# Performance work log

Hardware: AMD Instinct MI355X
Metric: run time of the kernel (lower is better)

## Reference

```python
import jax, jax.numpy as jnp
import numpy as np

# dims
B, T1, T2, SEG = 4, 16, 16, 4          # batch, src len, tgt len, max segment length
V, E, H, ENC = 8000, 256, 256, 512     # vocab, embed, lstm hidden, encoder units
EOS = 2                                 # end-of-segment symbol ($)
NEG = -1e30                             # finite -inf (grad-safe)


def setup_inputs():
    key = jax.random.key(0)
    ks = jax.random.split(key, 16)
    s = 0.05
    n = lambda k, shp: (jax.random.normal(k, shp) * s).astype(jnp.float32)
    return {
        "prev_output_tokens": jax.random.randint(ks[0], (B, T2), 0, V),
        "encoder_outs": jax.random.normal(ks[1], (T1, B, ENC), dtype=jnp.float32),
        "embed": n(ks[2], (V, E)),
        "start_embed": n(ks[3], (E,)),
        "proj_h_w": n(ks[4], (H, ENC)), "proj_h_b": jnp.zeros((H,), jnp.float32),
        "proj_c_w": n(ks[5], (H, ENC)), "proj_c_b": jnp.zeros((H,), jnp.float32),
        "w_ih0": n(ks[6], (4 * H, H + E)), "w_hh0": n(ks[7], (4 * H, H)), "b0": jnp.zeros((4 * H,), jnp.float32),
        "w_ih1": n(ks[8], (4 * H, H)), "w_hh1": n(ks[9], (4 * H, H)), "b1": jnp.zeros((4 * H,), jnp.float32),
        "fc_w": n(ks[10], (V, H)), "fc_b": jnp.zeros((V,), jnp.float32),
    }


def _lstm_cell(x, h, c, w_ih, w_hh, b):
    # PyTorch LSTMCell gate order: i, f, g, o
    g = x @ w_ih.T + h @ w_hh.T + b
    i, f, gg, o = jnp.split(g, 4, axis=-1)
    c_new = jax.nn.sigmoid(f) * c + jax.nn.sigmoid(i) * jnp.tanh(gg)
    h_new = jax.nn.sigmoid(o) * jnp.tanh(c_new)
    return h_new, c_new


def reference(prev_output_tokens, encoder_outs, embed, start_embed,
              proj_h_w, proj_h_b, proj_c_w, proj_c_b,
              w_ih0, w_hh0, b0, w_ih1, w_hh1, b1, fc_w, fc_b):
    y = prev_output_tokens                                     # [B, T2]
    # segment windows: tok[b, t2, k] = y[b, t2+k] (clipped; masked later via logpy mask)
    pos = jnp.arange(T2 + 1)[:, None] + jnp.arange(SEG)[None, :]   # [T2+1, SEG]
    tok = y[:, jnp.minimum(pos, T2 - 1)]                            # [B, T2+1, SEG]
    emb_tok = embed[tok]                                            # [B, T2+1, SEG, E]
    x0 = jnp.broadcast_to(start_embed, (B, T2 + 1, 1, E))
    xs = jnp.moveaxis(jnp.concatenate([x0, emb_tok], axis=2), 2, 0)  # [SEG+1, B, T2+1, E]
    tgt = jnp.concatenate([tok, jnp.zeros((B, T2 + 1, 1), tok.dtype)], axis=2)
    tgt = jnp.moveaxis(tgt, 2, 0)                                    # [SEG+1, B, T2+1]

    # per-encoder-position initial states / context (encoder proj, as in __init__)
    eo = jnp.swapaxes(encoder_outs, 0, 1)                            # [B, T1, ENC]
    h0 = eo @ proj_h_w.T + proj_h_b                                  # [B, T1, H]
    c0 = eo @ proj_c_w.T + proj_c_b
    ctx = jnp.broadcast_to(h0[:, :, None, :], (B, T1, T2 + 1, H))

    def step(carry, inp):
        h1, c1, h2, c2 = carry
        x, t = inp                                                   # x [B,T2+1,E], t [B,T2+1]
        xb = jnp.broadcast_to(x[:, None, :, :], (B, T1, T2 + 1, E))
        h1, c1 = _lstm_cell(jnp.concatenate([ctx, xb], axis=-1), h1, c1, w_ih0, w_hh0, b0)
        h2, c2 = _lstm_cell(h1, h2, c2, w_ih1, w_hh1, b1)
        logp = jax.nn.log_softmax(h2 @ fc_w.T + fc_b, axis=-1)       # [B,T1,T2+1,V]
        idx = jnp.broadcast_to(t[:, None, :, None], (B, T1, T2 + 1, 1))
        sel = jnp.take_along_axis(logp, idx, axis=-1)[..., 0]
        return (h1, c1, h2, c2), (sel, logp[..., EOS])

    carry0 = (ctx,
              jnp.broadcast_to(c0[:, :, None, :], (B, T1, T2 + 1, H)),
              jnp.zeros((B, T1, T2 + 1, H), jnp.float32),
              jnp.zeros((B, T1, T2 + 1, H), jnp.float32))
    _, (sel, eosp) = jax.lax.scan(step, carry0, (xs, tgt))           # each [SEG+1,B,T1,T2+1]

    # logpy[b,t1,t2,j] = sum_{k<j} logp_k(y[t2+k]) + logp_j(EOS)
    cum = jnp.concatenate([jnp.zeros((1, B, T1, T2 + 1), sel.dtype),
                           jnp.cumsum(sel[:SEG], axis=0)], axis=0)
    logpy = jnp.moveaxis(cum + eosp, 0, -1)                          # [B,T1,T2+1,SEG+1]
    jmask = (jnp.arange(T2 + 1)[:, None] + jnp.arange(SEG + 1)[None, :]) <= T2
    logpy = jnp.where(jmask[None, None], logpy, NEG)

    # semi-Markov forward DP: alpha[t1+1, t2] = LSE_j alpha[t1, t2-j] + logpy[t1, t2-j, j]
    alpha0 = jnp.full((B, T2 + 1), NEG, sel.dtype).at[:, 0].set(0.0)

    def dp(alpha, row):                                              # row [B, T2+1, SEG+1]
        v = alpha[:, :, None] + row
        shifted = jnp.stack(
            [jnp.pad(v[:, :T2 + 1 - j, j], ((0, 0), (j, 0)), constant_values=NEG)
             for j in range(SEG + 1)], axis=0)
        return jax.nn.logsumexp(shifted, axis=0), None

    alpha, _ = jax.lax.scan(dp, alpha0, jnp.moveaxis(logpy, 1, 0))
    return alpha[:, T2]                                              # log-likelihood per batch elem
```

## Files before the change

kernel.cpp:

```cpp
#include <hip/hip_runtime.h>
#include <math.h>

#define B 4
#define T1 16
#define T2 16
#define SEG 4
#define V 8000
#define E 256
#define H 256
#define ENC 512
#define EOS 2
#define NEGV -1e30f
#define G4 1024
#define NCELL 1088
#define T21 17
#define NL 272
#define MP 5504
#define NTM 43
#define NTN 63
#define NFCT (NTM*NTN)
#define NPART 126

typedef __attribute__((ext_vector_type(4))) float f32x4;
typedef __attribute__((ext_vector_type(8))) short bf16x8;

__device__ __forceinline__ float sigm(float x) { return 1.f / (1.f + __expf(-x)); }
__device__ __forceinline__ float ftanh(float x) { float e = __expf(2.f * x); return 1.f - 2.f / (e + 1.f); }
__device__ __forceinline__ float b2f(short x) {
    unsigned u = ((unsigned)(unsigned short)x) << 16;
    return __builtin_bit_cast(float, u);
}
__device__ __forceinline__ short f2b(float f) {
    unsigned u = __builtin_bit_cast(unsigned, f);
    unsigned r = (u + 0x7fffu + ((u >> 16) & 1u)) >> 16;
    return (short)r;
}

__device__ __forceinline__ int swz8(int row) { return (row & 7) ^ ((row & 3) << 1); }

__device__ __forceinline__ void stage64(const char* g0, size_t gstrideB, int kOffB, char* lds) {
    int tid = threadIdx.x;
#pragma unroll
    for (int it = 0; it < 8; ++it) {
        int chunk = it * 256 + tid;
        int row = chunk >> 5;
        int g = chunk & 31;
        const char* src = g0 + (size_t)row * gstrideB + kOffB + ((g ^ swz8(row)) << 4);
        __builtin_amdgcn_global_load_lds((const __attribute__((address_space(1))) void*)src,
                                         (__attribute__((address_space(3))) void*)(lds + chunk * 16),
                                         16, 0, 0);
    }
}
__device__ __forceinline__ bf16x8 lds_frag(const char* lds, int row, int col16) {
    return *(const bf16x8*)(lds + row * 512 + ((col16 ^ swz8(row)) << 4));
}
__device__ __forceinline__ void mma_tile(const char* smA, const char* smB,
                                         int wave, int ln, int kg, f32x4 acc[4]) {
#pragma unroll
    for (int ks = 0; ks < 8; ++ks) {
        bf16x8 a = lds_frag(smA, wave * 16 + ln, ks * 4 + kg);
#pragma unroll
        for (int nf = 0; nf < 4; ++nf) {
            bf16x8 b = lds_frag(smB, nf * 16 + ln, ks * 4 + kg);
            acc[nf] = __builtin_amdgcn_mfma_f32_16x16x32_bf16(a, b, acc[nf], 0, 0, 0);
        }
    }
}

__device__ __forceinline__ bf16x8 frag128(const char* lds, int row, int gl) {
    return *(const bf16x8*)(lds + row * 256 + ((gl ^ swz8(row)) << 4));
}

__global__ void k_setup(const float* __restrict__ fcw, const float* __restrict__ whh0,
                        const float* __restrict__ wih1, const float* __restrict__ whh1,
                        const float* __restrict__ phw, const float* __restrict__ pcw,
                        const float* __restrict__ wih0, const float* __restrict__ b1,
                        short* __restrict__ fcwbf, short* __restrict__ whh0i, short* __restrict__ w1i,
                        float* __restrict__ projhT, float* __restrict__ projcT,
                        float* __restrict__ ctxT, float* __restrict__ xT, float* __restrict__ b1i) {
    int bid = blockIdx.x, tid = threadIdx.x;
    if (bid < 2000) {
        int i = (bid * 256 + tid) * 4;
        float4 v = *(const float4*)&fcw[i];
        short4 o = { f2b(v.x), f2b(v.y), f2b(v.z), f2b(v.w) };
        *(short4*)&fcwbf[i] = o;
        return;
    }
    bid -= 2000;
    if (bid < 256) {
        int i = (bid * 256 + tid) * 4;
        int gp = i >> 8, k = i & 255;
        float4 v = *(const float4*)&whh0[(size_t)((gp & 3) * 256 + (gp >> 2)) * 256 + k];
        short4 o = { f2b(v.x), f2b(v.y), f2b(v.z), f2b(v.w) };
        *(short4*)&whh0i[i] = o;
        return;
    }
    bid -= 256;
    if (bid < 512) {
        int i = (bid * 256 + tid) * 4;
        int gp = i >> 9, k = i & 511;
        int g = (gp & 3) * 256 + (gp >> 2);
        const float* src = (k < 256) ? &wih1[(size_t)g * 256 + k] : &whh1[(size_t)g * 256 + (k - 256)];
        float4 v = *(const float4*)src;
        short4 o = { f2b(v.x), f2b(v.y), f2b(v.z), f2b(v.w) };
        *(short4*)&w1i[i] = o;
        return;
    }
    bid -= 512;
    if (bid < 128) {
        int i = (bid * 256 + tid) * 4;
        int k = i >> 8, r = i & 255;
        float4 o = { phw[(size_t)r * ENC + k], phw[(size_t)(r + 1) * ENC + k],
                     phw[(size_t)(r + 2) * ENC + k], phw[(size_t)(r + 3) * ENC + k] };
        *(float4*)&projhT[i] = o;
        return;
    }
    bid -= 128;
    if (bid < 128) {
        int i = (bid * 256 + tid) * 4;
        int k = i >> 8, r = i & 255;
        float4 o = { pcw[(size_t)r * ENC + k], pcw[(size_t)(r + 1) * ENC + k],
                     pcw[(size_t)(r + 2) * ENC + k], pcw[(size_t)(r + 3) * ENC + k] };
        *(float4*)&projcT[i] = o;
        return;
    }
    bid -= 128;
    if (bid < 512) {
        int i = (bid * 256 + tid) * 4;
        int g = i >> 9, k = i & 511;
        float4 v = *(const float4*)&wih0[i];
        float* base = (k < 256) ? &ctxT[(size_t)k * G4 + g] : &xT[(size_t)(k - 256) * G4 + g];
        base[0] = v.x; base[G4] = v.y; base[2 * G4] = v.z; base[3 * G4] = v.w;
        return;
    }
    bid -= 512;
    if (bid < 1) {
        float4 o = { b1[tid], b1[256 + tid], b1[512 + tid], b1[768 + tid] };
        *(float4*)&b1i[tid * 4] = o;
        return;
    }
}

__global__ void k_init_state(const float* __restrict__ enc, const float* __restrict__ phT,
                             const float* __restrict__ phb, const float* __restrict__ pcT,
                             const float* __restrict__ pcb, float* __restrict__ h0, float* __restrict__ c0) {
    __shared__ float eo[ENC];
    int bi = blockIdx.x;
    int b = bi / T1, i = bi % T1;
    int j = threadIdx.x;
    for (int e = j; e < ENC; e += 256) eo[e] = enc[(size_t)(i * B + b) * ENC + e];
    __syncthreads();
    float ha = phb[j], ca = pcb[j];
    for (int e = 0; e < ENC; ++e) {
        float x = eo[e];
        ha += x * phT[(size_t)e * H + j];
        ca += x * pcT[(size_t)e * H + j];
    }
    h0[(size_t)bi * H + j] = ha;
    c0[(size_t)bi * H + j] = ca;
}

__global__ void k_init2(const int* __restrict__ y, const float* __restrict__ embed, const float* __restrict__ se,
                        const float* __restrict__ h0, const float* __restrict__ c0,
                        const float* __restrict__ ctxT, const float* __restrict__ xT,
                        const float* __restrict__ b0,
                        float* __restrict__ c1, float* __restrict__ c2,
                        short* __restrict__ hcA, short* __restrict__ hcB,
                        float* __restrict__ pre_ctxi, float* __restrict__ pre_xi) {
    __shared__ float sb[256];
    int bid = blockIdx.x, j = threadIdx.x;
    if (bid < NCELL) {
        int cell = bid, bi = cell / T21;
        c1[(size_t)cell * H + j] = c0[(size_t)bi * H + j];
        c2[(size_t)cell * H + j] = 0.f;
        hcA[(size_t)cell * 512 + j] = f2b(h0[(size_t)bi * H + j]);
        hcB[(size_t)cell * 512 + 256 + j] = 0;
        return;
    }
    bid -= NCELL;
    if (bid < 64) {
        int bi = bid;
        sb[j] = h0[(size_t)bi * H + j];
        __syncthreads();
        float a0 = b0[j], a1 = b0[256 + j], a2 = b0[512 + j], a3 = b0[768 + j];
        for (int k = 0; k < H; ++k) {
            float x = sb[k];
            const float* w = ctxT + (size_t)k * G4;
            a0 += x * w[j]; a1 += x * w[256 + j]; a2 += x * w[512 + j]; a3 += x * w[768 + j];
        }
        *(float4*)&pre_ctxi[(size_t)bi * G4 + 4 * j] = make_float4(a0, a1, a2, a3);
        return;
    }
    bid -= 64;
    int row = bid;
    int s = row / (B * T21), rem = row % (B * T21);
    int b = rem / T21, t = rem % T21;
    const float* src;
    if (s == 0) src = se;
    else { int tt = t + s - 1; if (tt > 15) tt = 15; src = embed + (size_t)y[b * T2 + tt] * E; }
    sb[j] = src[j];
    __syncthreads();
    float a0 = 0, a1 = 0, a2 = 0, a3 = 0;
    for (int k = 0; k < E; ++k) {
        float x = sb[k];
        const float* w = xT + (size_t)k * G4;
        a0 += x * w[j]; a1 += x * w[256 + j]; a2 += x * w[512 + j]; a3 += x * w[768 + j];
    }
    *(float4*)&pre_xi[(size_t)row * G4 + 4 * j] = make_float4(a0, a1, a2, a3);
}

__device__ __forceinline__ void lstm0_body(int step, int l, char* smA, char* smB,
        const short* __restrict__ IN, const short* __restrict__ whh0i,
        const float* __restrict__ pre_ctxi, const float* __restrict__ pre_xi,
        float* __restrict__ c1, short* __restrict__ OUT) {
    int tid = threadIdx.x;
    int wave = tid >> 6, lane = tid & 63, ln = lane & 15, kg = lane >> 4;
    int mb = l >> 4, nb = l & 15;
    int m0 = mb * 64, n0 = nb * 64;
    stage64((const char*)(IN + (size_t)m0 * 512), 1024, 0, smA);
    stage64((const char*)(whh0i + (size_t)n0 * 256), 512, 0, smB);
    __syncthreads();
    f32x4 acc[4] = {};
    mma_tile(smA, smB, wave, ln, kg, acc);
    __syncthreads();
    float* sg = (float*)smA;
#pragma unroll
    for (int nf = 0; nf < 4; ++nf)
#pragma unroll
        for (int r = 0; r < 4; ++r)
            sg[(wave * 16 + kg * 4 + r) * 68 + nf * 16 + ln] = acc[nf][r];
    __syncthreads();
    int jlo = nb * 16;
#pragma unroll
    for (int q2 = 0; q2 < 4; ++q2) {
        int item = q2 * 256 + tid;
        int c = item >> 4, jj = item & 15;
        int cell = m0 + c;
        int j = jlo + jj;
        float4 g = *(float4*)&sg[c * 68 + 4 * jj];
        int bi = cell / T21;
        int bb = bi >> 4;
        int t = cell % T21;
        int prow = (step * B + bb) * T21 + t;
        float4 pc = *(const float4*)&pre_ctxi[(size_t)bi * G4 + 4 * j];
        float4 px = *(const float4*)&pre_xi[(size_t)prow * G4 + 4 * j];
        float ig = g.x + pc.x + px.x, fg = g.y + pc.y + px.y;
        float gg = g.z + pc.z + px.z, og = g.w + pc.w + px.w;
        float cold = c1[(size_t)cell * H + j];
        float cn = sigm(fg) * cold + sigm(ig) * ftanh(gg);
        float hn = sigm(og) * ftanh(cn);
        c1[(size_t)cell * H + j] = cn;
        OUT[(size_t)cell * 512 + j] = f2b(hn);
    }
}

__device__ __forceinline__ void lstm1_body(int l, char* smA, char* smB,
        const short* __restrict__ IN, const short* __restrict__ w1i,
        const float* __restrict__ b1i, float* __restrict__ c2,
        short* __restrict__ slab, short* __restrict__ OUT) {
    int tid = threadIdx.x;
    int wave = tid >> 6, lane = tid & 63, ln = lane & 15, kg = lane >> 4;
    int mb = l >> 4, nb = l & 15;
    int m0 = mb * 64, n0 = nb * 64;
    f32x4 acc[4] = {};
#pragma unroll
    for (int kh = 0; kh < 2; ++kh) {
        if (kh) __syncthreads();
        stage64((const char*)(IN + (size_t)m0 * 512), 1024, kh * 512, smA);
        stage64((const char*)(w1i + (size_t)n0 * 512), 1024, kh * 512, smB);
        __syncthreads();
        mma_tile(smA, smB, wave, ln, kg, acc);
    }
    __syncthreads();
    float* sg = (float*)smA;
#pragma unroll
    for (int nf = 0; nf < 4; ++nf)
#pragma unroll
        for (int r = 0; r < 4; ++r)
            sg[(wave * 16 + kg * 4 + r) * 68 + nf * 16 + ln] = acc[nf][r];
    __syncthreads();
    int jlo = nb * 16;
#pragma unroll
    for (int q2 = 0; q2 < 4; ++q2) {
        int item = q2 * 256 + tid;
        int c = item >> 4, jj = item & 15;
        int cell = m0 + c;
        int j = jlo + jj;
        float4 g = *(float4*)&sg[c * 68 + 4 * jj];
        float4 bv = *(const float4*)&b1i[4 * j];
        float ig = g.x + bv.x, fg = g.y + bv.y, gg = g.z + bv.z, og = g.w + bv.w;
        float cold = c2[(size_t)cell * H + j];
        float cn = sigm(fg) * cold + sigm(ig) * ftanh(gg);
        float hn = sigm(og) * ftanh(cn);
        c2[(size_t)cell * H + j] = cn;
        short hb = f2b(hn);
        slab[(size_t)cell * 256 + j] = hb;
        OUT[(size_t)cell * 512 + 256 + j] = hb;
    }
}

__global__ __launch_bounds__(256, 2) void k_lstm(int s, int n_l1,
        const short* __restrict__ IN, short* __restrict__ OUT, short* __restrict__ slab,
        const short* __restrict__ whh0i, const short* __restrict__ w1i,
        const float* __restrict__ pre_ctxi, const float* __restrict__ pre_xi,
        const float* __restrict__ b1i, float* __restrict__ c1, float* __restrict__ c2) {
    __shared__ char smem[65536];
    char* smA = smem;
    char* smB = smem + 32768;
    int bx = blockIdx.x;
    if (bx < n_l1) lstm1_body(bx, smA, smB, IN, w1i, b1i, c2, slab, OUT);
    else lstm0_body(s + 1, bx - n_l1, smA, smB, IN, whh0i, pre_ctxi, pre_xi, c1, OUT);
}

__global__ __launch_bounds__(256, 2) void k_fc(const short* __restrict__ h2base, const short* __restrict__ Wv,
        const float* __restrict__ fcb, float* __restrict__ psum) {
    __shared__ char smem[65536];
    char* smA = smem;
    char* smB = smem + 32768;
    int bx = blockIdx.x;
    int xcd = bx & 7, idx = bx >> 3;
    int q = NFCT >> 3, r = NFCT & 7;
    int tl = xcd * q + (xcd < r ? xcd : r) + idx;
    int nb = tl / NTM, mb = tl % NTM;
    int m0 = mb * 128, n0 = nb * 128;
    int tid = threadIdx.x;
    int wave = tid >> 6, lane = tid & 63, ln = lane & 15, kg = lane >> 4;
    int wm = wave >> 1, wn = wave & 1;
    f32x4 acc[4][4] = {};
#pragma unroll
    for (int kh = 0; kh < 2; ++kh) {
        if (kh) __syncthreads();
#pragma unroll
        for (int it = 0; it < 8; ++it) {
            int chunk = it * 256 + tid;
            int row = chunk >> 4;
            int g = chunk & 15;
            const char* src = (const char*)(h2base + (size_t)(m0 + row) * 256)
                              + kh * 256 + ((g ^ swz8(row)) << 4);
            __builtin_amdgcn_global_load_lds((const __attribute__((address_space(1))) void*)src,
                                             (__attribute__((address_space(3))) void*)(smA + chunk * 16),
                                             16, 0, 0);
        }
#pragma unroll
        for (int it = 0; it < 8; ++it) {
            int chunk = it * 256 + tid;
            int row = chunk >> 4;
            int g = chunk & 15;
            int grow = n0 + row; if (grow > V - 1) grow = V - 1;
            const char* src = (const char*)(Wv + (size_t)grow * 256)
                              + kh * 256 + ((g ^ swz8(row)) << 4);
            __builtin_amdgcn_global_load_lds((const __attribute__((address_space(1))) void*)src,
                                             (__attribute__((address_space(3))) void*)(smB + chunk * 16),
                                             16, 0, 0);
        }
        __syncthreads();
#pragma unroll
        for (int ks = 0; ks < 4; ++ks) {
            bf16x8 a[4], b[4];
#pragma unroll
            for (int mf = 0; mf < 4; ++mf) a[mf] = frag128(smA, wm * 64 + mf * 16 + ln, ks * 4 + kg);
#pragma unroll
            for (int nf = 0; nf < 4; ++nf) b[nf] = frag128(smB, wn * 64 + nf * 16 + ln, ks * 4 + kg);
#pragma unroll
            for (int mf = 0; mf < 4; ++mf)
#pragma unroll
                for (int nf = 0; nf < 4; ++nf)
                    acc[mf][nf] = __builtin_amdgcn_mfma_f32_16x16x32_bf16(a[mf], b[nf], acc[mf][nf], 0, 0, 0);
        }
    }
    float rs[4][4];
#pragma unroll
    for (int mf = 0; mf < 4; ++mf)
#pragma unroll
        for (int r2 = 0; r2 < 4; ++r2) rs[mf][r2] = 0.f;
#pragma unroll
    for (int nf = 0; nf < 4; ++nf) {
        int col = n0 + wn * 64 + nf * 16 + ln;
        float fbn = (col < V) ? fcb[col] : NEGV;
#pragma unroll
        for (int mf = 0; mf < 4; ++mf)
#pragma unroll
            for (int r2 = 0; r2 < 4; ++r2)
                rs[mf][r2] += __expf(acc[mf][nf][r2] + fbn);
    }
#pragma unroll
    for (int mask = 1; mask < 16; mask <<= 1)
#pragma unroll
        for (int mf = 0; mf < 4; ++mf)
#pragma unroll
            for (int r2 = 0; r2 < 4; ++r2)
                rs[mf][r2] += __shfl_xor(rs[mf][r2], mask);
    if (ln == 0) {
#pragma unroll
        for (int mf = 0; mf < 4; ++mf)
#pragma unroll
            for (int r2 = 0; r2 < 4; ++r2)
                psum[(size_t)(nb * 2 + wn) * MP + m0 + wm * 64 + mf * 16 + kg * 4 + r2] = rs[mf][r2];
    }
}

__global__ void k_combine(const short* __restrict__ h2all, const short* __restrict__ Wv,
        const float* __restrict__ fcb, const int* __restrict__ y,
        const float* __restrict__ psum, float* __restrict__ sel, float* __restrict__ eosp) {
    int cb = blockIdx.x;
    int s = cb / 17, blk = cb % 17;
    int tid = threadIdx.x;
    int cl = tid >> 2, q = tid & 3;
    int cell = blk * 64 + cl;
    int b = cell / (T1 * T21);
    int t = cell % T21;
    int tv = 0;
    if (s < SEG) { int tt = t + s; if (tt > 15) tt = 15; tv = y[b * T2 + tt]; }
    const short* hp = h2all + (size_t)(s + 1) * NCELL * 256 + (size_t)cell * 256 + q * 64;
    const short* w1 = Wv + (size_t)tv * 256 + q * 64;
    const short* w2 = Wv + (size_t)EOS * 256 + q * 64;
    float d1 = 0.f, d2 = 0.f;
#pragma unroll
    for (int u = 0; u < 8; ++u) {
        bf16x8 av  = *(const bf16x8*)(hp + u * 8);
        bf16x8 wv1 = *(const bf16x8*)(w1 + u * 8);
        bf16x8 wv2 = *(const bf16x8*)(w2 + u * 8);
#pragma unroll
        for (int e = 0; e < 8; ++e) {
            float a = b2f(av[e]);
            d1 += a * b2f(wv1[e]);
            d2 += a * b2f(wv2[e]);
        }
    }
    d1 += __shfl_xor(d1, 1); d1 += __shfl_xor(d1, 2);
    d2 += __shfl_xor(d2, 1); d2 += __shfl_xor(d2, 2);
    int col = s * NCELL + cell;
    float ss = 0.f;
    for (int v2 = q * 32; v2 < q * 32 + 32 && v2 < NPART; ++v2)
        ss += psum[(size_t)v2 * MP + col];
    ss += __shfl_xor(ss, 1); ss += __shfl_xor(ss, 2);
    if (q == 0) {
        float lse = __logf(ss);
        sel[s * NCELL + cell]  = d1 + fcb[tv]  - lse;
        eosp[s * NCELL + cell] = d2 + fcb[EOS] - lse;
    }
}

__global__ void k_dp(const float* __restrict__ sel, const float* __restrict__ eosp, float* __restrict__ out) {
    __shared__ float row[SEG + 1][NCELL];
    __shared__ float alpha[B][T21];
    int tid = threadIdx.x;
    for (int c = tid; c < NCELL; c += 256) {
        float cum = 0.f;
        row[0][c] = eosp[c];
#pragma unroll
        for (int j = 1; j <= SEG; ++j) {
            cum += sel[(j - 1) * NCELL + c];
            row[j][c] = cum + eosp[j * NCELL + c];
        }
    }
    int b = tid / T21, t = tid % T21;
    bool act = tid < B * T21;
    if (act) alpha[b][t] = (t == 0) ? 0.f : NEGV;
    __syncthreads();
    for (int i = 0; i < T1; ++i) {
        float val = NEGV;
        if (act) {
            float terms[SEG + 1];
            float mx = -3.4e38f;
            int cnt2 = 0;
            for (int j = 0; j <= SEG && j <= t; ++j) {
                int cell = (b * T1 + i) * T21 + (t - j);
                float term = alpha[b][t - j] + row[j][cell];
                terms[cnt2++] = term;
                mx = fmaxf(mx, term);
            }
            float ssum = 0.f;
            for (int k2 = 0; k2 < cnt2; ++k2) ssum += __expf(terms[k2] - mx);
            val = mx + __logf(ssum);
        }
        __syncthreads();
        if (act) alpha[b][t] = val;
        __syncthreads();
    }
    if (act && t == T2) out[b] = alpha[b][T2];
}

extern "C" void kernel_launch(void* const* d_in, const int* in_sizes, int n_in,
                              void* d_out, int out_size, void* d_ws, size_t ws_size,
                              hipStream_t stream) {
    const int*   y     = (const int*)d_in[0];
    const float* enc   = (const float*)d_in[1];
    const float* embed = (const float*)d_in[2];
    const float* se    = (const float*)d_in[3];
    const float* phw   = (const float*)d_in[4];
    const float* phb   = (const float*)d_in[5];
    const float* pcw   = (const float*)d_in[6];
    const float* pcb   = (const float*)d_in[7];
    const float* wih0  = (const float*)d_in[8];
    const float* whh0  = (const float*)d_in[9];
    const float* b0    = (const float*)d_in[10];
    const float* wih1  = (const float*)d_in[11];
    const float* whh1  = (const float*)d_in[12];
    const float* b1    = (const float*)d_in[13];
    const float* fcw   = (const float*)d_in[14];
    const float* fcb   = (const float*)d_in[15];

    float* ws = (float*)d_ws;
    size_t off = 0;
    auto alloc = [&](size_t n) { float* p = ws + off; off += n; return p; };
    float* projhT   = alloc((size_t)ENC * H);
    float* projcT   = alloc((size_t)ENC * H);
    float* ctxT     = alloc((size_t)H * G4);
    float* xT       = alloc((size_t)E * G4);
    float* h0       = alloc((size_t)B * T1 * H);
    float* c0       = alloc((size_t)B * T1 * H);
    float* pre_ctxi = alloc((size_t)B * T1 * G4);
    float* pre_xi   = alloc((size_t)(SEG + 1) * B * T21 * G4);
    float* c1       = alloc((size_t)NCELL * H);
    float* c2       = alloc((size_t)NCELL * H);
    float* b1i      = alloc((size_t)G4);
    float* selbuf   = alloc((size_t)(SEG + 1) * NCELL);
    float* eospbuf  = alloc((size_t)(SEG + 1) * NCELL);
    float* psum     = alloc((size_t)NPART * MP);
    short* hc0      = (short*)alloc((size_t)NCELL * 512 / 2);
    short* hc1      = (short*)alloc((size_t)NCELL * 512 / 2);
    short* h2all    = (short*)alloc(((size_t)6 * NCELL + 64) * 256 / 2);
    short* whh0i    = (short*)alloc((size_t)G4 * 256 / 2);
    short* w1i      = (short*)alloc((size_t)G4 * 512 / 2);
    short* fcwbf    = (short*)alloc((size_t)V * H / 2);

    hipLaunchKernelGGL(k_setup, dim3(3537), dim3(256), 0, stream,
                       fcw, whh0, wih1, whh1, phw, pcw, wih0, b1,
                       fcwbf, whh0i, w1i, projhT, projcT, ctxT, xT, b1i);
    hipLaunchKernelGGL(k_init_state, dim3(B * T1), dim3(256), 0, stream,
                       enc, projhT, phb, projcT, pcb, h0, c0);
    hipLaunchKernelGGL(k_init2, dim3(NCELL + 64 + (SEG + 1) * B * T21), dim3(256), 0, stream,
                       y, embed, se, h0, c0, ctxT, xT, b0, c1, c2, hc0, hc1,
                       pre_ctxi, pre_xi);

    short* hcb[2] = { hc0, hc1 };
    hipLaunchKernelGGL(k_lstm, dim3(NL), dim3(256), 0, stream,
                       -1, 0, hcb[0], hcb[1], h2all,
                       whh0i, w1i, pre_ctxi, pre_xi, b1i, c1, c2);
    for (int s = 0; s < SEG; ++s) {
        hipLaunchKernelGGL(k_lstm, dim3(2 * NL), dim3(256), 0, stream,
                           s, NL, hcb[(s + 1) & 1], hcb[s & 1],
                           h2all + (size_t)(s + 1) * NCELL * 256,
                           whh0i, w1i, pre_ctxi, pre_xi, b1i, c1, c2);
    }
    hipLaunchKernelGGL(k_lstm, dim3(NL), dim3(256), 0, stream,
                       4, NL, hcb[1], hcb[0],
                       h2all + (size_t)5 * NCELL * 256,
                       whh0i, w1i, pre_ctxi, pre_xi, b1i, c1, c2);

    hipLaunchKernelGGL(k_fc, dim3(NFCT), dim3(256), 0, stream,
                       h2all + (size_t)NCELL * 256, fcwbf, fcb, psum);
    hipLaunchKernelGGL(k_combine, dim3(85), dim3(256), 0, stream,
                       h2all, fcwbf, fcb, y, psum, selbuf, eospbuf);
    hipLaunchKernelGGL(k_dp, dim3(1), dim3(256), 0, stream, selbuf, eospbuf, (float*)d_out);
}
```

Before: 186.6 us.

## Halve LSTM tile M, shrink LDS, split init projection across more blocks

The LSTM step kernels now use 32-row M tiles instead of 64, doubling the block count. Each wave computes a 16x32 sub-tile, LDS is cut to 48KB, and launch bounds allow 3 blocks per CU, all aimed at better occupancy on a small grid. The FC kernel stages K in 128-byte quarters so it needs only 32KB of LDS and can run 4 blocks per CU. The encoder projection is split into 4 K-partitions merged into the existing init kernels, removing a serial 64-block launch, and the final LSTM step skips a dead OUT write. In exchange, weight tiles are restaged twice as often and there are more synchronisation rounds.

```diff
diff --git a/kernel.cpp b/kernel.cpp
--- a/kernel.cpp
+++ b/kernel.cpp
@@ -14,7 +14,7 @@
 #define G4 1024
 #define NCELL 1088
 #define T21 17
-#define NL 272
+#define NLT 544
 #define MP 5504
 #define NTM 43
 #define NTN 63
@@ -35,13 +35,13 @@
     unsigned r = (u + 0x7fffu + ((u >> 16) & 1u)) >> 16;
     return (short)r;
 }
-
 __device__ __forceinline__ int swz8(int row) { return (row & 7) ^ ((row & 3) << 1); }
 
-__device__ __forceinline__ void stage64(const char* g0, size_t gstrideB, int kOffB, char* lds) {
+template<int ISSUES>
+__device__ __forceinline__ void stage512(const char* g0, size_t gstrideB, int kOffB, char* lds) {
     int tid = threadIdx.x;
 #pragma unroll
-    for (int it = 0; it < 8; ++it) {
+    for (int it = 0; it < ISSUES; ++it) {
         int chunk = it * 256 + tid;
         int row = chunk >> 5;
         int g = chunk & 31;
@@ -51,24 +51,9 @@
                                          16, 0, 0);
     }
 }
-__device__ __forceinline__ bf16x8 lds_frag(const char* lds, int row, int col16) {
-    return *(const bf16x8*)(lds + row * 512 + ((col16 ^ swz8(row)) << 4));
-}
-__device__ __forceinline__ void mma_tile(const char* smA, const char* smB,
-                                         int wave, int ln, int kg, f32x4 acc[4]) {
-#pragma unroll
-    for (int ks = 0; ks < 8; ++ks) {
-        bf16x8 a = lds_frag(smA, wave * 16 + ln, ks * 4 + kg);
-#pragma unroll
-        for (int nf = 0; nf < 4; ++nf) {
-            bf16x8 b = lds_frag(smB, nf * 16 + ln, ks * 4 + kg);
-            acc[nf] = __builtin_amdgcn_mfma_f32_16x16x32_bf16(a, b, acc[nf], 0, 0, 0);
-        }
-    }
-}
-
-__device__ __forceinline__ bf16x8 frag128(const char* lds, int row, int gl) {
-    return *(const bf16x8*)(lds + row * 256 + ((gl ^ swz8(row)) << 4));
+template<int RSB>
+__device__ __forceinline__ bf16x8 fragT(const char* lds, int row, int g) {
+    return *(const bf16x8*)(lds + row * RSB + ((g ^ swz8(row)) << 4));
 }
 
 __global__ void k_setup(const float* __restrict__ fcw, const float* __restrict__ whh0,
@@ -137,62 +122,33 @@
     if (bid < 1) {
         float4 o = { b1[tid], b1[256 + tid], b1[512 + tid], b1[768 + tid] };
         *(float4*)&b1i[tid * 4] = o;
-        return;
-    }
-}
-
-__global__ void k_init_state(const float* __restrict__ enc, const float* __restrict__ phT,
-                             const float* __restrict__ phb, const float* __restrict__ pcT,
-                             const float* __restrict__ pcb, float* __restrict__ h0, float* __restrict__ c0) {
-    __shared__ float eo[ENC];
-    int bi = blockIdx.x;
-    int b = bi / T1, i = bi % T1;
-    int j = threadIdx.x;
-    for (int e = j; e < ENC; e += 256) eo[e] = enc[(size_t)(i * B + b) * ENC + e];
-    __syncthreads();
-    float ha = phb[j], ca = pcb[j];
-    for (int e = 0; e < ENC; ++e) {
-        float x = eo[e];
-        ha += x * phT[(size_t)e * H + j];
-        ca += x * pcT[(size_t)e * H + j];
-    }
-    h0[(size_t)bi * H + j] = ha;
-    c0[(size_t)bi * H + j] = ca;
-}
-
-__global__ void k_init2(const int* __restrict__ y, const float* __restrict__ embed, const float* __restrict__ se,
-                        const float* __restrict__ h0, const float* __restrict__ c0,
-                        const float* __restrict__ ctxT, const float* __restrict__ xT,
-                        const float* __restrict__ b0,
-                        float* __restrict__ c1, float* __restrict__ c2,
-                        short* __restrict__ hcA, short* __restrict__ hcB,
-                        float* __restrict__ pre_ctxi, float* __restrict__ pre_xi) {
+    }
+}
+
+__global__ void k_init1(const int* __restrict__ y, const float* __restrict__ embed, const float* __restrict__ se,
+                        const float* __restrict__ enc, const float* __restrict__ phT,
+                        const float* __restrict__ phb, const float* __restrict__ pcT,
+                        const float* __restrict__ pcb, const float* __restrict__ xT,
+                        float* __restrict__ h0p, float* __restrict__ c0p, float* __restrict__ pre_xi) {
     __shared__ float sb[256];
     int bid = blockIdx.x, j = threadIdx.x;
-    if (bid < NCELL) {
-        int cell = bid, bi = cell / T21;
-        c1[(size_t)cell * H + j] = c0[(size_t)bi * H + j];
-        c2[(size_t)cell * H + j] = 0.f;
-        hcA[(size_t)cell * 512 + j] = f2b(h0[(size_t)bi * H + j]);
-        hcB[(size_t)cell * 512 + 256 + j] = 0;
-        return;
-    }
-    bid -= NCELL;
-    if (bid < 64) {
-        int bi = bid;
-        sb[j] = h0[(size_t)bi * H + j];
+    if (bid < 256) {
+        int q = bid & 3, bi = bid >> 2;
+        int b = bi / T1, i = bi % T1;
+        if (j < 128) sb[j] = enc[(size_t)(i * B + b) * ENC + q * 128 + j];
         __syncthreads();
-        float a0 = b0[j], a1 = b0[256 + j], a2 = b0[512 + j], a3 = b0[768 + j];
-        for (int k = 0; k < H; ++k) {
-            float x = sb[k];
-            const float* w = ctxT + (size_t)k * G4;
-            a0 += x * w[j]; a1 += x * w[256 + j]; a2 += x * w[512 + j]; a3 += x * w[768 + j];
-        }
-        *(float4*)&pre_ctxi[(size_t)bi * G4 + 4 * j] = make_float4(a0, a1, a2, a3);
-        return;
-    }
-    bid -= 64;
-    int row = bid;
+        float ha = (q == 0) ? phb[j] : 0.f;
+        float ca = (q == 0) ? pcb[j] : 0.f;
+        for (int e = 0; e < 128; ++e) {
+            float x = sb[e];
+            ha += x * phT[(size_t)(q * 128 + e) * H + j];
+            ca += x * pcT[(size_t)(q * 128 + e) * H + j];
+        }
+        h0p[(size_t)(q * 64 + bi) * H + j] = ha;
+        c0p[(size_t)(q * 64 + bi) * H + j] = ca;
+        return;
+    }
+    int row = bid - 256;
     int s = row / (B * T21), rem = row % (B * T21);
     int b = rem / T21, t = rem % T21;
     const float* src;
@@ -209,30 +165,80 @@
     *(float4*)&pre_xi[(size_t)row * G4 + 4 * j] = make_float4(a0, a1, a2, a3);
 }
 
+__global__ void k_init2(const float* __restrict__ h0p, const float* __restrict__ c0p,
+                        const float* __restrict__ ctxT, const float* __restrict__ b0,
+                        float* __restrict__ c1, float* __restrict__ c2,
+                        short* __restrict__ hcA, short* __restrict__ hcB,
+                        float* __restrict__ pre_ctxi) {
+    __shared__ float sb[256];
+    int bid = blockIdx.x, j = threadIdx.x;
+    if (bid < NCELL) {
+        int cell = bid, bi = cell / T21;
+        float hv = 0.f, cv = 0.f;
+#pragma unroll
+        for (int q = 0; q < 4; ++q) {
+            hv += h0p[(size_t)(q * 64 + bi) * H + j];
+            cv += c0p[(size_t)(q * 64 + bi) * H + j];
+        }
+        c1[(size_t)cell * H + j] = cv;
+        c2[(size_t)cell * H + j] = 0.f;
+        hcA[(size_t)cell * 512 + j] = f2b(hv);
+        hcB[(size_t)cell * 512 + 256 + j] = 0;
+        return;
+    }
+    int bi = bid - NCELL;
+    float hv = 0.f;
+#pragma unroll
+    for (int q = 0; q < 4; ++q) hv += h0p[(size_t)(q * 64 + bi) * H + j];
+    sb[j] = hv;
+    __syncthreads();
+    float a0 = b0[j], a1 = b0[256 + j], a2 = b0[512 + j], a3 = b0[768 + j];
+    for (int k = 0; k < H; ++k) {
+        float x = sb[k];
+        const float* w = ctxT + (size_t)k * G4;
+        a0 += x * w[j]; a1 += x * w[256 + j]; a2 += x * w[512 + j]; a3 += x * w[768 + j];
+    }
+    *(float4*)&pre_ctxi[(size_t)bi * G4 + 4 * j] = make_float4(a0, a1, a2, a3);
+}
+
+__device__ __forceinline__ void mma32(const char* smA, const char* smB,
+                                      int wm, int wn2, int ln, int kg, f32x4 acc[2]) {
+#pragma unroll
+    for (int ks = 0; ks < 8; ++ks) {
+        bf16x8 a = fragT<512>(smA, wm * 16 + ln, ks * 4 + kg);
+#pragma unroll
+        for (int nf = 0; nf < 2; ++nf) {
+            bf16x8 b = fragT<512>(smB, wn2 * 32 + nf * 16 + ln, ks * 4 + kg);
+            acc[nf] = __builtin_amdgcn_mfma_f32_16x16x32_bf16(a, b, acc[nf], 0, 0, 0);
+        }
+    }
+}
+
 __device__ __forceinline__ void lstm0_body(int step, int l, char* smA, char* smB,
         const short* __restrict__ IN, const short* __restrict__ whh0i,
         const float* __restrict__ pre_ctxi, const float* __restrict__ pre_xi,
         float* __restrict__ c1, short* __restrict__ OUT) {
     int tid = threadIdx.x;
     int wave = tid >> 6, lane = tid & 63, ln = lane & 15, kg = lane >> 4;
+    int wm = wave & 1, wn2 = wave >> 1;
     int mb = l >> 4, nb = l & 15;
-    int m0 = mb * 64, n0 = nb * 64;
-    stage64((const char*)(IN + (size_t)m0 * 512), 1024, 0, smA);
-    stage64((const char*)(whh0i + (size_t)n0 * 256), 512, 0, smB);
-    __syncthreads();
-    f32x4 acc[4] = {};
-    mma_tile(smA, smB, wave, ln, kg, acc);
+    int m0 = mb * 32, n0 = nb * 64;
+    stage512<4>((const char*)(IN + (size_t)m0 * 512), 1024, 0, smA);
+    stage512<8>((const char*)(whh0i + (size_t)n0 * 256), 512, 0, smB);
+    __syncthreads();
+    f32x4 acc[2] = {};
+    mma32(smA, smB, wm, wn2, ln, kg, acc);
     __syncthreads();
     float* sg = (float*)smA;
 #pragma unroll
-    for (int nf = 0; nf < 4; ++nf)
+    for (int nf = 0; nf < 2; ++nf)
 #pragma unroll
         for (int r = 0; r < 4; ++r)
-            sg[(wave * 16 + kg * 4 + r) * 68 + nf * 16 + ln] = acc[nf][r];
+            sg[(wm * 16 + kg * 4 + r) * 68 + wn2 * 32 + nf * 16 + ln] = acc[nf][r];
     __syncthreads();
     int jlo = nb * 16;
 #pragma unroll
-    for (int q2 = 0; q2 < 4; ++q2) {
+    for (int q2 = 0; q2 < 2; ++q2) {
         int item = q2 * 256 + tid;
         int c = item >> 4, jj = item & 15;
         int cell = m0 + c;
@@ -257,31 +263,32 @@
 __device__ __forceinline__ void lstm1_body(int l, char* smA, char* smB,
         const short* __restrict__ IN, const short* __restrict__ w1i,
         const float* __restrict__ b1i, float* __restrict__ c2,
-        short* __restrict__ slab, short* __restrict__ OUT) {
+        short* __restrict__ slab, short* __restrict__ OUT, bool writeOUT) {
     int tid = threadIdx.x;
     int wave = tid >> 6, lane = tid & 63, ln = lane & 15, kg = lane >> 4;
+    int wm = wave & 1, wn2 = wave >> 1;
     int mb = l >> 4, nb = l & 15;
-    int m0 = mb * 64, n0 = nb * 64;
-    f32x4 acc[4] = {};
+    int m0 = mb * 32, n0 = nb * 64;
+    f32x4 acc[2] = {};
 #pragma unroll
     for (int kh = 0; kh < 2; ++kh) {
         if (kh) __syncthreads();
-        stage64((const char*)(IN + (size_t)m0 * 512), 1024, kh * 512, smA);
-        stage64((const char*)(w1i + (size_t)n0 * 512), 1024, kh * 512, smB);
+        stage512<4>((const char*)(IN + (size_t)m0 * 512), 1024, kh * 512, smA);
+        stage512<8>((const char*)(w1i + (size_t)n0 * 512), 1024, kh * 512, smB);
         __syncthreads();
-        mma_tile(smA, smB, wave, ln, kg, acc);
+        mma32(smA, smB, wm, wn2, ln, kg, acc);
     }
     __syncthreads();
     float* sg = (float*)smA;
 #pragma unroll
-    for (int nf = 0; nf < 4; ++nf)
+    for (int nf = 0; nf < 2; ++nf)
 #pragma unroll
         for (int r = 0; r < 4; ++r)
-            sg[(wave * 16 + kg * 4 + r) * 68 + nf * 16 + ln] = acc[nf][r];
+            sg[(wm * 16 + kg * 4 + r) * 68 + wn2 * 32 + nf * 16 + ln] = acc[nf][r];
     __syncthreads();
     int jlo = nb * 16;
 #pragma unroll
-    for (int q2 = 0; q2 < 4; ++q2) {
+    for (int q2 = 0; q2 < 2; ++q2) {
         int item = q2 * 256 + tid;
         int c = item >> 4, jj = item & 15;
         int cell = m0 + c;
@@ -295,28 +302,28 @@
         c2[(size_t)cell * H + j] = cn;
         short hb = f2b(hn);
         slab[(size_t)cell * 256 + j] = hb;
-        OUT[(size_t)cell * 512 + 256 + j] = hb;
-    }
-}
-
-__global__ __launch_bounds__(256, 2) void k_lstm(int s, int n_l1,
+        if (writeOUT) OUT[(size_t)cell * 512 + 256 + j] = hb;
+    }
+}
+
+__global__ __launch_bounds__(256, 3) void k_lstm(int s, int n_l1, int wout,
         const short* __restrict__ IN, short* __restrict__ OUT, short* __restrict__ slab,
         const short* __restrict__ whh0i, const short* __restrict__ w1i,
         const float* __restrict__ pre_ctxi, const float* __restrict__ pre_xi,
         const float* __restrict__ b1i, float* __restrict__ c1, float* __restrict__ c2) {
-    __shared__ char smem[65536];
+    __shared__ __align__(16) char smem[49152];
     char* smA = smem;
-    char* smB = smem + 32768;
+    char* smB = smem + 16384;
     int bx = blockIdx.x;
-    if (bx < n_l1) lstm1_body(bx, smA, smB, IN, w1i, b1i, c2, slab, OUT);
+    if (bx < n_l1) lstm1_body(bx, smA, smB, IN, w1i, b1i, c2, slab, OUT, wout != 0);
     else lstm0_body(s + 1, bx - n_l1, smA, smB, IN, whh0i, pre_ctxi, pre_xi, c1, OUT);
 }
 
-__global__ __launch_bounds__(256, 2) void k_fc(const short* __restrict__ h2base, const short* __restrict__ Wv,
+__global__ __launch_bounds__(256, 4) void k_fc(const short* __restrict__ h2base, const short* __restrict__ Wv,
         const float* __restrict__ fcb, float* __restrict__ psum) {
-    __shared__ char smem[65536];
+    __shared__ __align__(16) char smem[32768];
     char* smA = smem;
-    char* smB = smem + 32768;
+    char* smB = smem + 16384;
     int bx = blockIdx.x;
     int xcd = bx & 7, idx = bx >> 3;
     int q = NFCT >> 3, r = NFCT & 7;
@@ -328,39 +335,39 @@
     int wm = wave >> 1, wn = wave & 1;
     f32x4 acc[4][4] = {};
 #pragma unroll
-    for (int kh = 0; kh < 2; ++kh) {
-        if (kh) __syncthreads();
-#pragma unroll
-        for (int it = 0; it < 8; ++it) {
+    for (int kq = 0; kq < 4; ++kq) {
+        if (kq) __syncthreads();
+#pragma unroll
+        for (int it = 0; it < 4; ++it) {
             int chunk = it * 256 + tid;
-            int row = chunk >> 4;
-            int g = chunk & 15;
+            int row = chunk >> 3;
+            int g = chunk & 7;
             const char* src = (const char*)(h2base + (size_t)(m0 + row) * 256)
-                              + kh * 256 + ((g ^ swz8(row)) << 4);
+                              + kq * 128 + ((g ^ swz8(row)) << 4);
             __builtin_amdgcn_global_load_lds((const __attribute__((address_space(1))) void*)src,
                                              (__attribute__((address_space(3))) void*)(smA + chunk * 16),
                                              16, 0, 0);
         }
 #pragma unroll
-        for (int it = 0; it < 8; ++it) {
+        for (int it = 0; it < 4; ++it) {
             int chunk = it * 256 + tid;
-            int row = chunk >> 4;
-            int g = chunk & 15;
+            int row = chunk >> 3;
+            int g = chunk & 7;
             int grow = n0 + row; if (grow > V - 1) grow = V - 1;
             const char* src = (const char*)(Wv + (size_t)grow * 256)
-                              + kh * 256 + ((g ^ swz8(row)) << 4);
+                              + kq * 128 + ((g ^ swz8(row)) << 4);
             __builtin_amdgcn_global_load_lds((const __attribute__((address_space(1))) void*)src,
                                              (__attribute__((address_space(3))) void*)(smB + chunk * 16),
                                              16, 0, 0);
         }
         __syncthreads();
 #pragma unroll
-        for (int ks = 0; ks < 4; ++ks) {
+        for (int ks = 0; ks < 2; ++ks) {
             bf16x8 a[4], b[4];
 #pragma unroll
-            for (int mf = 0; mf < 4; ++mf) a[mf] = frag128(smA, wm * 64 + mf * 16 + ln, ks * 4 + kg);
-#pragma unroll
-            for (int nf = 0; nf < 4; ++nf) b[nf] = frag128(smB, wn * 64 + nf * 16 + ln, ks * 4 + kg);
+            for (int mf = 0; mf < 4; ++mf) a[mf] = fragT<128>(smA, wm * 64 + mf * 16 + ln, ks * 4 + kg);
+#pragma unroll
+            for (int nf = 0; nf < 4; ++nf) b[nf] = fragT<128>(smB, wn * 64 + nf * 16 + ln, ks * 4 + kg);
 #pragma unroll
             for (int mf = 0; mf < 4; ++mf)
 #pragma unroll
@@ -508,8 +515,8 @@
     float* projcT   = alloc((size_t)ENC * H);
     float* ctxT     = alloc((size_t)H * G4);
     float* xT       = alloc((size_t)E * G4);
-    float* h0       = alloc((size_t)B * T1 * H);
-    float* c0       = alloc((size_t)B * T1 * H);
+    float* h0p      = alloc((size_t)4 * 64 * H);
+    float* c0p      = alloc((size_t)4 * 64 * H);
     float* pre_ctxi = alloc((size_t)B * T1 * G4);
     float* pre_xi   = alloc((size_t)(SEG + 1) * B * T21 * G4);
     float* c1       = alloc((size_t)NCELL * H);
@@ -528,24 +535,23 @@
     hipLaunchKernelGGL(k_setup, dim3(3537), dim3(256), 0, stream,
                        fcw, whh0, wih1, whh1, phw, pcw, wih0, b1,
                        fcwbf, whh0i, w1i, projhT, projcT, ctxT, xT, b1i);
-    hipLaunchKernelGGL(k_init_state, dim3(B * T1), dim3(256), 0, stream,
-                       enc, projhT, phb, projcT, pcb, h0, c0);
-    hipLaunchKernelGGL(k_init2, dim3(NCELL + 64 + (SEG + 1) * B * T21), dim3(256), 0, stream,
-                       y, embed, se, h0, c0, ctxT, xT, b0, c1, c2, hc0, hc1,
-                       pre_ctxi, pre_xi);
+    hipLaunchKernelGGL(k_init1, dim3(256 + (SEG + 1) * B * T21), dim3(256), 0, stream,
+                       y, embed, se, enc, projhT, phb, projcT, pcb, xT, h0p, c0p, pre_xi);
+    hipLaunchKernelGGL(k_init2, dim3(NCELL + 64), dim3(256), 0, stream,
+                       h0p, c0p, ctxT, b0, c1, c2, hc0, hc1, pre_ctxi);
 
     short* hcb[2] = { hc0, hc1 };
-    hipLaunchKernelGGL(k_lstm, dim3(NL), dim3(256), 0, stream,
-                       -1, 0, hcb[0], hcb[1], h2all,
+    hipLaunchKernelGGL(k_lstm, dim3(NLT), dim3(256), 0, stream,
+                       -1, 0, 1, hcb[0], hcb[1], h2all,
                        whh0i, w1i, pre_ctxi, pre_xi, b1i, c1, c2);
     for (int s = 0; s < SEG; ++s) {
-        hipLaunchKernelGGL(k_lstm, dim3(2 * NL), dim3(256), 0, stream,
-                           s, NL, hcb[(s + 1) & 1], hcb[s & 1],
+        hipLaunchKernelGGL(k_lstm, dim3(2 * NLT), dim3(256), 0, stream,
+                           s, NLT, 1, hcb[(s + 1) & 1], hcb[s & 1],
                            h2all + (size_t)(s + 1) * NCELL * 256,
                            whh0i, w1i, pre_ctxi, pre_xi, b1i, c1, c2);
     }
-    hipLaunchKernelGGL(k_lstm, dim3(NL), dim3(256), 0, stream,
-                       4, NL, hcb[1], hcb[0],
+    hipLaunchKernelGGL(k_lstm, dim3(NLT), dim3(256), 0, stream,
+                       4, NLT, 0, hcb[1], hcb[0],
                        h2all + (size_t)5 * NCELL * 256,
                        whh0i, w1i, pre_ctxi, pre_xi, b1i, c1, c2);
 
```

Result: faster. 173.6 us (-7.0%).
